# Kernel optimization log

Measured on AMD Instinct MI355X. Metric: run time of the kernel, lower is better.

The kernel has to match this reference:

```python
import jax, jax.numpy as jnp
import numpy as np

NUM_EMBEDDINGS = 1024
EMBEDDING_DIM = 256
BETA = 0.25


def setup_inputs() -> dict:
    key = jax.random.key(0)
    k1, k2 = jax.random.split(key)
    inputs = jax.random.normal(k1, (32, EMBEDDING_DIM, 64, 64), dtype=jnp.float32)
    # codebook init: uniform(-1/K, 1/K), matching nn.Embedding init in the module
    embedding = jax.random.uniform(
        k2, (NUM_EMBEDDINGS, EMBEDDING_DIM), dtype=jnp.float32,
        minval=-1.0 / NUM_EMBEDDINGS, maxval=1.0 / NUM_EMBEDDINGS)
    return {"inputs": inputs, "embedding": embedding, "beta": BETA}


def reference(inputs, embedding, beta):
    # inputs: [B, D, H, W] -> [B, H, W, D]
    x = jnp.transpose(inputs, (0, 2, 3, 1))
    in_shape = x.shape
    flat = x.reshape(-1, embedding.shape[1])  # [N, D]
    dist = (jnp.sum(flat * flat, axis=1, keepdims=True)
            + jnp.sum(embedding * embedding, axis=1)
            - 2.0 * flat @ embedding.T)
    codebook_indices = jnp.argmin(dist, axis=1)  # [N]
    quantized = embedding[codebook_indices].reshape(in_shape)  # [B,H,W,D]
    sg = jax.lax.stop_gradient
    e_latent_loss = beta * jnp.mean((sg(quantized) - x) ** 2)
    q_latent_loss = jnp.mean((quantized - sg(x)) ** 2)
    loss = e_latent_loss + q_latent_loss
    # straight-through estimator
    quantized_st = x + sg(quantized - x)
    return loss, jnp.transpose(quantized_st, (0, 3, 1, 2))
```

## Files before the change

kernel.cpp:

```cpp
#include <hip/hip_runtime.h>
#include <hip/hip_bf16.h>


#define DIN 256
#define NCODES 1024
#define NTOT 33554432

typedef __attribute__((ext_vector_type(8))) short short8;
typedef __attribute__((ext_vector_type(4))) float float4v;
typedef __attribute__((ext_vector_type(4))) unsigned short ushort4v;

static __device__ __forceinline__ unsigned short f2bf(float f) {
  unsigned int u = __float_as_uint(f);
  unsigned int r = (u + 0x7fffu + ((u >> 16) & 1u)) >> 16;
  return (unsigned short)r;
}

__global__ void vq_prep(const float* __restrict__ e,
                        unsigned short* __restrict__ e_bf,
                        float* __restrict__ norms) {
  int wave = threadIdx.x >> 6, lane = threadIdx.x & 63;
  int k = blockIdx.x * 4 + wave;
  const float4v* src = (const float4v*)(e + k * DIN);
  float4v v = src[lane];
  float ss = v[0]*v[0] + v[1]*v[1] + v[2]*v[2] + v[3]*v[3];
  ushort4v pk;
  pk[0] = f2bf(v[0]); pk[1] = f2bf(v[1]); pk[2] = f2bf(v[2]); pk[3] = f2bf(v[3]);
  ((ushort4v*)(e_bf + k * DIN))[lane] = pk;
  #pragma unroll
  for (int m = 1; m < 64; m <<= 1) ss += __shfl_xor(ss, m, 64);
  if (lane == 0) norms[k] = ss;
}

__global__ void __launch_bounds__(256, 2)
vq_main(const float* __restrict__ xin, const float* __restrict__ e_fp,
        const unsigned short* __restrict__ e_bf, const float* __restrict__ norms,
        float* __restrict__ out, float* __restrict__ loss_acc) {
  __shared__ char smem[65536];
  unsigned short* xs = (unsigned short*)smem;
  unsigned short* es = (unsigned short*)smem;
  float* vs  = (float*)(smem + 49152);
  int*   is_ = (int*)  (smem + 49664);
  int*   fi  = (int*)  (smem + 50176);
  float* rs  = (float*)(smem + 50432);
  float* qs  = (float*)smem;

  const int tid  = threadIdx.x;
  const int wave = tid >> 6, lane = tid & 63;
  const int m16  = lane & 15, quad = lane >> 4;
  const int wr   = wave >> 1, wc = wave & 1;
  const int b    = blockIdx.x >> 6, h = blockIdx.x & 63;
  const int base = b * 1048576 + h * 64;

  {
    int w = lane;
    for (int q8 = 0; q8 < 8; ++q8) {
      int cc = q8 * 4 + wave;
      int d0 = cc * 8;
      short8 pk;
      #pragma unroll
      for (int ii = 0; ii < 8; ++ii) {
        float xv = xin[base + (d0 + ii) * 4096 + w];
        pk[ii] = (short)f2bf(xv);
      }
      *(short8*)(xs + w * 256 + 8 * (cc ^ (w & 7))) = pk;
    }
  }
  __syncthreads();

  short8 areg[16];
  #pragma unroll
  for (int i = 0; i < 2; ++i) {
    #pragma unroll
    for (int kk = 0; kk < 8; ++kk) {
      int r = wr * 32 + i * 16 + m16;
      int cc = kk * 4 + quad;
      areg[i * 8 + kk] = *(short8*)(xs + r * 256 + 8 * (cc ^ (r & 7)));
    }
  }
  __syncthreads();

  float bestv[2][4];
  int   besti[2][4];
  float4v acc[2][4];
  #pragma unroll
  for (int i = 0; i < 2; ++i)
    #pragma unroll
    for (int r = 0; r < 4; ++r) {
      bestv[i][r] = INFINITY; besti[i][r] = 0;
      acc[i][r] = (float4v)(0.0f);
    }

  for (int ct = 0; ct < 8; ++ct) {
    int c0 = ct * 128;
    #pragma unroll
    for (int j = 0; j < 16; ++j) {
      int f = j * 256 + tid;
      int kL = f >> 5, cc = f & 31;
      short8 vch = *(const short8*)(e_bf + (c0 + kL) * 256 + cc * 8);
      *(short8*)(es + kL * 256 + 8 * (cc ^ (kL & 7))) = vch;
    }
    __syncthreads();
    #pragma unroll
    for (int kk = 0; kk < 8; ++kk) {
      short8 bfr[4];
      #pragma unroll
      for (int j = 0; j < 4; ++j) {
        int cL = wc * 64 + j * 16 + m16;
        int cc = kk * 4 + quad;
        bfr[j] = *(short8*)(es + cL * 256 + 8 * (cc ^ (cL & 7)));
      }
      #pragma unroll
      for (int i = 0; i < 2; ++i)
        #pragma unroll
        for (int j = 0; j < 4; ++j)
          acc[i][j] = __builtin_amdgcn_mfma_f32_16x16x32_bf16(
              areg[i * 8 + kk], bfr[j], acc[i][j], 0, 0, 0);
    }
    #pragma unroll
    for (int j = 0; j < 4; ++j) {
      int col = c0 + wc * 64 + j * 16 + m16;
      float nj = norms[col];
      #pragma unroll
      for (int i = 0; i < 2; ++i) {
        #pragma unroll
        for (int r = 0; r < 4; ++r) {
          float s = nj - 2.0f * acc[i][j][r];
          if (s < bestv[i][r]) { bestv[i][r] = s; besti[i][r] = col; }
        }
        acc[i][j] = (float4v)(0.0f);
      }
    }
    __syncthreads();
  }

  #pragma unroll
  for (int msk = 1; msk <= 8; msk <<= 1) {
    #pragma unroll
    for (int i = 0; i < 2; ++i)
      #pragma unroll
      for (int r = 0; r < 4; ++r) {
        float ov = __shfl_xor(bestv[i][r], msk, 64);
        int   oi = __shfl_xor(besti[i][r], msk, 64);
        if (ov < bestv[i][r] || (ov == bestv[i][r] && oi < besti[i][r])) {
          bestv[i][r] = ov; besti[i][r] = oi;
        }
      }
  }
  if (m16 == 0) {
    #pragma unroll
    for (int i = 0; i < 2; ++i)
      #pragma unroll
      for (int r = 0; r < 4; ++r) {
        int rl = wr * 32 + i * 16 + quad * 4 + r;
        vs [rl * 2 + wc] = bestv[i][r];
        is_[rl * 2 + wc] = besti[i][r];
      }
  }
  __syncthreads();
  if (tid < 64) {
    float v0 = vs[tid * 2], v1 = vs[tid * 2 + 1];
    fi[tid] = (v1 < v0) ? is_[tid * 2 + 1] : is_[tid * 2];
  }
  __syncthreads();

  float lsum = 0.0f;
  for (int h2 = 0; h2 < 2; ++h2) {
    #pragma unroll
    for (int j = 0; j < 8; ++j) {
      int f = j * 256 + tid;
      int w2 = f >> 5, cc = f & 31;
      int idx = fi[w2];
      float4v qv = *(const float4v*)(e_fp + idx * DIN + h2 * 128 + cc * 4);
      #pragma unroll
      for (int ii = 0; ii < 4; ++ii)
        qs[(cc * 4 + ii) * 65 + w2] = qv[ii];
    }
    __syncthreads();
    for (int dd = 0; dd < 32; ++dd) {
      int dL = wave * 32 + dd;
      int g = base + (h2 * 128 + dL) * 4096 + lane;
      float q  = qs[dL * 65 + lane];
      float xv = xin[g];
      out[1 + g] = q;
      float df = q - xv;
      lsum += df * df;
    }
    __syncthreads();
  }

  #pragma unroll
  for (int msk = 1; msk < 64; msk <<= 1) lsum += __shfl_xor(lsum, msk, 64);
  if (lane == 0) rs[wave] = lsum;
  __syncthreads();
  if (tid == 0) atomicAdd(loss_acc, rs[0] + rs[1] + rs[2] + rs[3]);
}

__global__ void vq_fin(const float* __restrict__ loss_acc,
                       const float* __restrict__ beta,
                       float* __restrict__ out) {
  out[0] = (1.0f + beta[0]) * loss_acc[0] / 33554432.0f;
}

extern "C" void kernel_launch(void* const* d_in, const int* in_sizes, int n_in,
                              void* d_out, int out_size, void* d_ws, size_t ws_size,
                              hipStream_t stream) {
  const float* xin  = (const float*)d_in[0];
  const float* emb  = (const float*)d_in[1];
  const float* beta = (const float*)d_in[2];
  float* out = (float*)d_out;
  float* loss_acc = (float*)d_ws;
  float* norms = (float*)((char*)d_ws + 4096);
  unsigned short* e_bf = (unsigned short*)((char*)d_ws + 8192);

  hipMemsetAsync(d_ws, 0, 4, stream);
  vq_prep<<<256, 256, 0, stream>>>(emb, e_bf, norms);
  vq_main<<<2048, 256, 0, stream>>>(xin, emb, e_bf, norms, out, loss_acc);
  vq_fin<<<1, 1, 0, stream>>>(loss_acc, beta, out);
}
```

Baseline: 365.5 us.

## Restructure VQ kernel: 512-thread blocks, async double-buffered codebook, loss from distances

The main kernel now processes four image rows per 512-thread block. Each wave owns 32 pixels against all codes, and the codebook streams through double-buffered 32-code tiles via global_load_lds. vq_prep pre-swizzles the bf16 codebook into the tile layout. The loss is computed from best distance plus the ||x||^2 norm instead of re-reading x, and quantized output uses vectorized float4 stores through a swizzled LDS transpose. This is meant to cut the x re-read and hide codebook load latency, at the cost of a bf16-approximated loss and more code complexity.

New measurement: 359.8 us. About the same (-1.6%).

```diff
diff --git a/kernel.cpp b/kernel.cpp
--- a/kernel.cpp
+++ b/kernel.cpp
@@ -1,10 +1,7 @@
 #include <hip/hip_runtime.h>
-#include <hip/hip_bf16.h>
 
 
 #define DIN 256
-#define NCODES 1024
-#define NTOT 33554432
 
 typedef __attribute__((ext_vector_type(8))) short short8;
 typedef __attribute__((ext_vector_type(4))) float float4v;
@@ -17,7 +14,7 @@
 }
 
 __global__ void vq_prep(const float* __restrict__ e,
-                        unsigned short* __restrict__ e_bf,
+                        unsigned short* __restrict__ e_pre,
                         float* __restrict__ norms) {
   int wave = threadIdx.x >> 6, lane = threadIdx.x & 63;
   int k = blockIdx.x * 4 + wave;
@@ -26,112 +23,136 @@
   float ss = v[0]*v[0] + v[1]*v[1] + v[2]*v[2] + v[3]*v[3];
   ushort4v pk;
   pk[0] = f2bf(v[0]); pk[1] = f2bf(v[1]); pk[2] = f2bf(v[2]); pk[3] = f2bf(v[3]);
-  ((ushort4v*)(e_bf + k * DIN))[lane] = pk;
+  int t = k >> 5, kL = k & 31;
+  int cc = lane >> 1, half = lane & 1;
+  int s = cc ^ (kL & 7);
+  *(ushort4v*)(e_pre + t * 8192 + kL * 256 + s * 8 + half * 4) = pk;
   #pragma unroll
   for (int m = 1; m < 64; m <<= 1) ss += __shfl_xor(ss, m, 64);
   if (lane == 0) norms[k] = ss;
 }
 
-__global__ void __launch_bounds__(256, 2)
+#define BARRIER_RAW() do { asm volatile("" ::: "memory"); \
+  __builtin_amdgcn_s_barrier(); asm volatile("" ::: "memory"); } while (0)
+
+__global__ void __launch_bounds__(512, 4)
 vq_main(const float* __restrict__ xin, const float* __restrict__ e_fp,
-        const unsigned short* __restrict__ e_bf, const float* __restrict__ norms,
+        const unsigned short* __restrict__ e_pre,
+        const float* __restrict__ norms,
         float* __restrict__ out, float* __restrict__ loss_acc) {
-  __shared__ char smem[65536];
+  __shared__ char smem[41024];
   unsigned short* xs = (unsigned short*)smem;
-  unsigned short* es = (unsigned short*)smem;
-  float* vs  = (float*)(smem + 49152);
-  int*   is_ = (int*)  (smem + 49664);
-  int*   fi  = (int*)  (smem + 50176);
-  float* rs  = (float*)(smem + 50432);
   float* qs  = (float*)smem;
+  float* nrm = (float*)(smem + 32768);
+  float* xnp = (float*)(smem + 36864);
+  int*   fi  = (int*)(smem + 38912);
+  float* xna = (float*)(smem + 39936);
+  float* prt = (float*)(smem + 40960);
 
   const int tid  = threadIdx.x;
   const int wave = tid >> 6, lane = tid & 63;
   const int m16  = lane & 15, quad = lane >> 4;
-  const int wr   = wave >> 1, wc = wave & 1;
-  const int b    = blockIdx.x >> 6, h = blockIdx.x & 63;
-  const int base = b * 1048576 + h * 64;
-
+  const int line0 = blockIdx.x * 4;
+
+  nrm[tid] = norms[tid];
+  nrm[tid + 512] = norms[tid + 512];
+
+  short8 areg[16];
+  const int wL  = wave >> 1;
+  const int w32 = (wave & 1) * 32;
   {
-    int w = lane;
-    for (int q8 = 0; q8 < 8; ++q8) {
-      int cc = q8 * 4 + wave;
-      int d0 = cc * 8;
-      short8 pk;
-      #pragma unroll
-      for (int ii = 0; ii < 8; ++ii) {
-        float xv = xin[base + (d0 + ii) * 4096 + w];
-        pk[ii] = (short)f2bf(xv);
-      }
-      *(short8*)(xs + w * 256 + 8 * (cc ^ (w & 7))) = pk;
-    }
-  }
-  __syncthreads();
-
-  short8 areg[16];
-  #pragma unroll
-  for (int i = 0; i < 2; ++i) {
-    #pragma unroll
-    for (int kk = 0; kk < 8; ++kk) {
-      int r = wr * 32 + i * 16 + m16;
-      int cc = kk * 4 + quad;
-      areg[i * 8 + kk] = *(short8*)(xs + r * 256 + 8 * (cc ^ (r & 7)));
+    const int w  = tid & 63;
+    const int cg = wave;
+    for (int L = 0; L < 4; ++L) {
+      int line = line0 + L;
+      const float* xl = xin + (line >> 6) * 1048576 + (line & 63) * 64;
+      __syncthreads();
+      float ss = 0.0f;
+      #pragma unroll
+      for (int q8 = 0; q8 < 4; ++q8) {
+        int cc = cg * 4 + q8;
+        short8 pk;
+        #pragma unroll
+        for (int ii = 0; ii < 8; ++ii) {
+          float xv = xl[(cc * 8 + ii) * 4096 + w];
+          ss += xv * xv;
+          pk[ii] = (short)f2bf(xv);
+        }
+        *(short8*)(xs + w * 256 + 8 * (cc ^ (w & 7))) = pk;
+      }
+      xnp[w * 8 + cg] = ss;
+      __syncthreads();
+      if (wL == L) {
+        #pragma unroll
+        for (int i = 0; i < 2; ++i)
+          #pragma unroll
+          for (int kk = 0; kk < 8; ++kk) {
+            int r = w32 + i * 16 + m16;
+            areg[i * 8 + kk] =
+                *(short8*)(xs + r * 256 + 8 * ((kk * 4 + quad) ^ (r & 7)));
+          }
+      }
+      if (tid < 64) {
+        float s2 = 0.0f;
+        #pragma unroll
+        for (int u = 0; u < 8; ++u) s2 += xnp[tid * 8 + u];
+        xna[L * 64 + tid] = s2;
+      }
     }
   }
   __syncthreads();
 
   float bestv[2][4];
   int   besti[2][4];
-  float4v acc[2][4];
   #pragma unroll
   for (int i = 0; i < 2; ++i)
     #pragma unroll
-    for (int r = 0; r < 4; ++r) {
-      bestv[i][r] = INFINITY; besti[i][r] = 0;
-      acc[i][r] = (float4v)(0.0f);
-    }
-
-  for (int ct = 0; ct < 8; ++ct) {
-    int c0 = ct * 128;
-    #pragma unroll
-    for (int j = 0; j < 16; ++j) {
-      int f = j * 256 + tid;
-      int kL = f >> 5, cc = f & 31;
-      short8 vch = *(const short8*)(e_bf + (c0 + kL) * 256 + cc * 8);
-      *(short8*)(es + kL * 256 + 8 * (cc ^ (kL & 7))) = vch;
-    }
-    __syncthreads();
-    #pragma unroll
-    for (int kk = 0; kk < 8; ++kk) {
-      short8 bfr[4];
-      #pragma unroll
-      for (int j = 0; j < 4; ++j) {
-        int cL = wc * 64 + j * 16 + m16;
-        int cc = kk * 4 + quad;
-        bfr[j] = *(short8*)(es + cL * 256 + 8 * (cc ^ (cL & 7)));
-      }
-      #pragma unroll
-      for (int i = 0; i < 2; ++i)
-        #pragma unroll
-        for (int j = 0; j < 4; ++j)
-          acc[i][j] = __builtin_amdgcn_mfma_f32_16x16x32_bf16(
-              areg[i * 8 + kk], bfr[j], acc[i][j], 0, 0, 0);
-    }
-    #pragma unroll
-    for (int j = 0; j < 4; ++j) {
-      int col = c0 + wc * 64 + j * 16 + m16;
-      float nj = norms[col];
-      #pragma unroll
-      for (int i = 0; i < 2; ++i) {
-        #pragma unroll
-        for (int r = 0; r < 4; ++r) {
-          float s = nj - 2.0f * acc[i][j][r];
-          if (s < bestv[i][r]) { bestv[i][r] = s; besti[i][r] = col; }
-        }
-        acc[i][j] = (float4v)(0.0f);
-      }
-    }
-    __syncthreads();
+    for (int r = 0; r < 4; ++r) { bestv[i][r] = INFINITY; besti[i][r] = 0; }
+
+  auto stage = [&](int t, int buf) {
+    const char* src = (const char*)e_pre + t * 16384;
+    char* dst = smem + buf * 16384;
+    #pragma unroll
+    for (int j = 0; j < 2; ++j) {
+      int off = (j * 8 + wave) * 1024 + lane * 16;
+      __builtin_amdgcn_global_load_lds(
+          (const __attribute__((address_space(1))) unsigned int*)(src + off),
+          (__attribute__((address_space(3))) unsigned int*)(dst + off),
+          16, 0, 0);
+    }
+  };
+
+  stage(0, 0);
+  for (int t = 0; t < 32; ++t) {
+    if (t < 31) {
+      stage(t + 1, (t + 1) & 1);
+      asm volatile("s_waitcnt vmcnt(2)" ::: "memory");
+    } else {
+      asm volatile("s_waitcnt vmcnt(0)" ::: "memory");
+    }
+    BARRIER_RAW();
+    const unsigned short* eb = (const unsigned short*)(smem + (t & 1) * 16384);
+    #pragma unroll
+    for (int j = 0; j < 2; ++j) {
+      int cL = j * 16 + m16;
+      float4v a0 = (float4v)(0.0f), a1 = (float4v)(0.0f);
+      #pragma unroll
+      for (int kk = 0; kk < 8; ++kk) {
+        short8 bfr = *(const short8*)(eb + cL * 256 + 8 * ((kk * 4 + quad) ^ (cL & 7)));
+        a0 = __builtin_amdgcn_mfma_f32_16x16x32_bf16(areg[kk],     bfr, a0, 0, 0, 0);
+        a1 = __builtin_amdgcn_mfma_f32_16x16x32_bf16(areg[8 + kk], bfr, a1, 0, 0, 0);
+      }
+      int col = t * 32 + cL;
+      float nj = nrm[col];
+      #pragma unroll
+      for (int r = 0; r < 4; ++r) {
+        float s0 = nj - 2.0f * a0[r];
+        if (s0 < bestv[0][r]) { bestv[0][r] = s0; besti[0][r] = col; }
+        float s1 = nj - 2.0f * a1[r];
+        if (s1 < bestv[1][r]) { bestv[1][r] = s1; besti[1][r] = col; }
+      }
+    }
+    BARRIER_RAW();
   }
 
   #pragma unroll
@@ -147,53 +168,57 @@
         }
       }
   }
+
+  float lsum = 0.0f;
   if (m16 == 0) {
     #pragma unroll
     for (int i = 0; i < 2; ++i)
       #pragma unroll
       for (int r = 0; r < 4; ++r) {
-        int rl = wr * 32 + i * 16 + quad * 4 + r;
-        vs [rl * 2 + wc] = bestv[i][r];
-        is_[rl * 2 + wc] = besti[i][r];
-      }
-  }
+        int row = wave * 32 + i * 16 + quad * 4 + r;
+        fi[row] = besti[i][r];
+        lsum += bestv[i][r] + xna[row];
+      }
+  }
+  #pragma unroll
+  for (int msk = 1; msk < 64; msk <<= 1) lsum += __shfl_xor(lsum, msk, 64);
+  if (lane == 0) prt[wave] = lsum;
   __syncthreads();
-  if (tid < 64) {
-    float v0 = vs[tid * 2], v1 = vs[tid * 2 + 1];
-    fi[tid] = (v1 < v0) ? is_[tid * 2 + 1] : is_[tid * 2];
-  }
-  __syncthreads();
-
-  float lsum = 0.0f;
-  for (int h2 = 0; h2 < 2; ++h2) {
-    #pragma unroll
-    for (int j = 0; j < 8; ++j) {
-      int f = j * 256 + tid;
-      int w2 = f >> 5, cc = f & 31;
-      int idx = fi[w2];
-      float4v qv = *(const float4v*)(e_fp + idx * DIN + h2 * 128 + cc * 4);
-      #pragma unroll
-      for (int ii = 0; ii < 4; ++ii)
-        qs[(cc * 4 + ii) * 65 + w2] = qv[ii];
-    }
-    __syncthreads();
-    for (int dd = 0; dd < 32; ++dd) {
-      int dL = wave * 32 + dd;
-      int g = base + (h2 * 128 + dL) * 4096 + lane;
-      float q  = qs[dL * 65 + lane];
-      float xv = xin[g];
-      out[1 + g] = q;
-      float df = q - xv;
-      lsum += df * df;
-    }
-    __syncthreads();
-  }
-
-  #pragma unroll
-  for (int msk = 1; msk < 64; msk <<= 1) lsum += __shfl_xor(lsum, msk, 64);
-  if (lane == 0) rs[wave] = lsum;
-  __syncthreads();
-  if (tid == 0) atomicAdd(loss_acc, rs[0] + rs[1] + rs[2] + rs[3]);
+  if (tid == 0) {
+    float s = 0.0f;
+    #pragma unroll
+    for (int u = 0; u < 8; ++u) s += prt[u];
+    atomicAdd(loss_acc, s);
+  }
+
+  for (int L = 0; L < 4; ++L) {
+    int line = line0 + L;
+    float* ob = out + 1 + (line >> 6) * 1048576 + (line & 63) * 64;
+    int w = tid >> 3, dg = tid & 7;
+    int idx = fi[L * 64 + w];
+    const float* er = e_fp + idx * 256;
+    int swz = (w >> 2) & 7;
+    for (int h2 = 0; h2 < 2; ++h2) {
+      #pragma unroll
+      for (int j = 0; j < 4; ++j) {
+        int c = dg + 8 * j;
+        float4v qv = *(const float4v*)(er + h2 * 128 + c * 4);
+        *(float4v*)(qs + w * 128 + (c ^ swz) * 4) = qv;
+      }
+      __syncthreads();
+      #pragma unroll
+      for (int it = 0; it < 4; ++it) {
+        int dl = it * 32 + wave * 4 + quad;
+        int slot = (dl >> 2) ^ (m16 & 7);
+        float4v ov;
+        #pragma unroll
+        for (int k = 0; k < 4; ++k)
+          ov[k] = qs[(m16 * 4 + k) * 128 + slot * 4 + (dl & 3)];
+        *(float4v*)(ob + (h2 * 128 + dl) * 4096 + m16 * 4) = ov;
+      }
+      __syncthreads();
+    }
+  }
 }
 
 __global__ void vq_fin(const float* __restrict__ loss_acc,
@@ -211,10 +236,10 @@
   float* out = (float*)d_out;
   float* loss_acc = (float*)d_ws;
   float* norms = (float*)((char*)d_ws + 4096);
-  unsigned short* e_bf = (unsigned short*)((char*)d_ws + 8192);
+  unsigned short* e_pre = (unsigned short*)((char*)d_ws + 8192);
 
   hipMemsetAsync(d_ws, 0, 4, stream);
-  vq_prep<<<256, 256, 0, stream>>>(emb, e_bf, norms);
-  vq_main<<<2048, 256, 0, stream>>>(xin, emb, e_bf, norms, out, loss_acc);
+  vq_prep<<<256, 256, 0, stream>>>(emb, e_pre, norms);
+  vq_main<<<512, 512, 0, stream>>>(xin, emb, e_pre, norms, out, loss_acc);
   vq_fin<<<1, 1, 0, stream>>>(loss_acc, beta, out);
 }
```
